# Kernel tuning notes

Measured on AMD Instinct MI355X. Metric: run time of the kernel, lower is better.

The kernel has to match this reference:

```python
import jax, jax.numpy as jnp
import numpy as np


def setup_inputs() -> dict:
    key = jax.random.key(0)
    k1, k2 = jax.random.split(key)
    B, C, H, W = 1, 128, 96, 128
    feat_l = jax.random.normal(k1, (B, C, H, W), dtype=jnp.float32)
    feat_r = jax.random.normal(k2, (B, C, H, W), dtype=jnp.float32)
    return {"feat_l": feat_l, "feat_r": feat_r, "scale_x": 4, "scale_y": 4}


def reference(feat_l, feat_r, scale_x, scale_y):
    B, C, H, W = feat_l.shape
    _, _, H_R, W_R = feat_r.shape
    # Full correlation volume: [B, H, W, H_R*W_R]  (the huge intermediate)
    corr = jnp.einsum('bchw,bcij->bhwij', feat_l, feat_r).reshape(B, H, W, H_R * W_R)
    flow_cost = jnp.max(corr, axis=3)           # [B, H, W]
    flat_idx = jnp.argmax(corr, axis=3)         # [B, H, W] int
    # Decode argmax index -> flow (u, v) relative to pixel grid
    xoff = jnp.arange(W)                        # [W]
    yoff = jnp.arange(H)                        # [H]
    u = -((flat_idx % W_R) * scale_x - xoff[None, None, :]).astype(jnp.float32)
    v = -((flat_idx // W_R) * scale_y - yoff[None, :, None]).astype(jnp.float32)
    flow = jnp.stack([u, v], axis=3)            # [B, H, W, 2]
    return flow, flow_cost
```

## Files before the change

### kernel.cpp

```cpp
#include <hip/hip_runtime.h>

#define K_TOT 128
#define H_DIM 96
#define W_DIM 128
#define M_TOT (H_DIM * W_DIM)
#define N_TOT (H_DIM * W_DIM)
#define SCALE 4
#define NEG_INF (-3.402823e38f)

#define KP 384
#define NH 24
#define SLAB_F16 24576

typedef _Float16 f16x8 __attribute__((ext_vector_type(8)));
typedef float f32x16 __attribute__((ext_vector_type(16)));

__global__ __launch_bounds__(256)
void split_prep_kernel(const float* __restrict__ L, const float* __restrict__ R,
                       _Float16* __restrict__ Ls, _Float16* __restrict__ Rs,
                       unsigned long long* __restrict__ keys) {
    const int t = threadIdx.x;
    if (blockIdx.x >= 1536) {
        int m = (blockIdx.x - 1536) * 256 + t;
        if (m < M_TOT) keys[m] = 0ull;
        return;
    }
    __shared__ __align__(16) _Float16 T[3][64][40];
    const int isR  = blockIdx.x >= 768;
    const int bb   = blockIdx.x - (isR ? 768 : 0);
    const int slab = bb >> 2;
    const int q    = bb & 3;
    const int P0   = slab * 64;
    const int kq   = q * 32;
    const float* src = isR ? R : L;
    _Float16* dst = isR ? Rs : Ls;

    const int p4 = (t & 15) * 4;
    const int k0 = t >> 4;
#pragma unroll
    for (int it = 0; it < 2; ++it) {
        const int kl = k0 + it * 16;
        float4 v = *(const float4*)&src[(size_t)(kq + kl) * M_TOT + P0 + p4];
        float xs[4] = {v.x, v.y, v.z, v.w};
#pragma unroll
        for (int j = 0; j < 4; ++j) {
            _Float16 h = (_Float16)xs[j];
            float hf = (float)h;
            float r = xs[j] - hf;
            T[0][p4 + j][kl] = h;
            T[1][p4 + j][kl] = (_Float16)(r * 64.0f);
            T[2][p4 + j][kl] = (_Float16)(hf * 0.015625f);
        }
    }
    __syncthreads();
#pragma unroll
    for (int it = 0; it < 3; ++it) {
        const int u   = it * 256 + t;
        const int col = u & 31;
        const int hi  = (u >> 5) & 1;
        const int op  = (u >> 6) & 1;
        const int jj  = (u >> 7) & 1;
        const int sec = u >> 8;
        const int half   = sec * 8 + 2 * q + jj;
        const int c      = half * 128 + op * 64 + hi * 32 + col;
        const int klocal = jj * 16 + hi * 8;
        const int plane  = (sec == 0) ? 0 : (isR ? sec : 3 - sec);
        const int row    = op * 32 + col;
        float4 v = *(const float4*)&T[plane][row][klocal];
        *(float4*)&dst[(size_t)slab * SLAB_F16 + (size_t)c * 8] = v;
    }
}

__global__ __launch_bounds__(256, 4)
void mfma_corr_kernel(const _Float16* __restrict__ Ls, const _Float16* __restrict__ Rs,
                      unsigned long long* __restrict__ keys) {
    __shared__ float vals[128 * 17];
    __shared__ int   idxs[128 * 17];

    const int tid  = threadIdx.x;
    const int lane = tid & 63;
    const int wid  = tid >> 6;
    const int wr   = wid >> 1;
    const int wc   = wid & 1;
    const int col  = lane & 31;
    const int hi   = lane >> 5;
    const int bid  = blockIdx.x;
    const int xcd  = bid & 7;
    const int b    = bid >> 3;
    const int mt   = b / 12;
    const int nt   = xcd * 12 + b % 12;
    const int m0   = mt * 128;
    const int n0   = nt * 128;

    const _Float16* pA = Ls + (size_t)(mt * 2 + wr) * SLAB_F16 + lane * 8;
    const _Float16* pB = Rs + (size_t)(nt * 2 + wc) * SLAB_F16 + lane * 8;

    f32x16 acc[2][2];
#pragma unroll
    for (int mi = 0; mi < 2; ++mi)
#pragma unroll
        for (int ni = 0; ni < 2; ++ni) acc[mi][ni] = (f32x16)(0.0f);

    f16x8 fA[3][2], fB[3][2];
#define LOADH(hh, s) {                                              \
        fA[s][0] = *(const f16x8*)(pA + (hh) * 1024);               \
        fA[s][1] = *(const f16x8*)(pA + (hh) * 1024 + 512);         \
        fB[s][0] = *(const f16x8*)(pB + (hh) * 1024);               \
        fB[s][1] = *(const f16x8*)(pB + (hh) * 1024 + 512);         \
    }
    LOADH(0, 0);
    LOADH(1, 1);
#pragma unroll
    for (int h = 0; h < NH; ++h) {
        if (h + 2 < NH) LOADH(h + 2, (h + 2) % 3);
        const int s = h % 3;
        __builtin_amdgcn_s_setprio(1);
        acc[0][0] = __builtin_amdgcn_mfma_f32_32x32x16_f16(fA[s][0], fB[s][0], acc[0][0], 0, 0, 0);
        acc[0][1] = __builtin_amdgcn_mfma_f32_32x32x16_f16(fA[s][0], fB[s][1], acc[0][1], 0, 0, 0);
        acc[1][0] = __builtin_amdgcn_mfma_f32_32x32x16_f16(fA[s][1], fB[s][0], acc[1][0], 0, 0, 0);
        acc[1][1] = __builtin_amdgcn_mfma_f32_32x32x16_f16(fA[s][1], fB[s][1], acc[1][1], 0, 0, 0);
        __builtin_amdgcn_s_setprio(0);
    }
#undef LOADH

#pragma unroll
    for (int mi = 0; mi < 2; ++mi) {
#pragma unroll
        for (int reg = 0; reg < 16; ++reg) {
            float best = acc[mi][0][reg];
            int bni = 0;
            if (acc[mi][1][reg] > best) { best = acc[mi][1][reg]; bni = 1; }
            int n = n0 + wc * 64 + bni * 32 + col;
#pragma unroll
            for (int d = 16; d >= 8; d >>= 1) {
                float ov = __shfl_xor(best, d, 64);
                int   oi = __shfl_xor(n, d, 64);
                if (ov > best || (ov == best && oi < n)) { best = ov; n = oi; }
            }
            if ((lane & 24) == 0) {
                const int row = wr * 64 + mi * 32 + (reg & 3) + 8 * (reg >> 2) + 4 * hi;
                const int c   = wc * 8 + (lane & 7);
                vals[row * 17 + c] = best;
                idxs[row * 17 + c] = n;
            }
        }
    }
    __syncthreads();
    if (tid < 128) {
        float bv = vals[tid * 17 + 0]; int bi = idxs[tid * 17 + 0];
#pragma unroll
        for (int c = 1; c < 16; ++c) {
            float v = vals[tid * 17 + c]; int ix = idxs[tid * 17 + c];
            if (v > bv || (v == bv && ix < bi)) { bv = v; bi = ix; }
        }
        unsigned vb = __float_as_uint(bv);
        vb = (vb & 0x80000000u) ? ~vb : (vb | 0x80000000u);
        unsigned long long key = ((unsigned long long)vb << 32) | (unsigned)(~bi);
        atomicMax(&keys[m0 + tid], key);
    }
}

__global__ void finalize_keys_kernel(const unsigned long long* __restrict__ keys,
                                     float* __restrict__ out) {
    int m = blockIdx.x * blockDim.x + threadIdx.x;
    if (m >= M_TOT) return;
    unsigned long long key = keys[m];
    unsigned hi = (unsigned)(key >> 32);
    unsigned bits = (hi & 0x80000000u) ? (hi & 0x7fffffffu) : ~hi;
    float v = __uint_as_float(bits);
    int idx = (int)(~(unsigned)(key & 0xffffffffu));
    int h = m / W_DIM, w = m % W_DIM;
    int i = idx / W_DIM, j = idx % W_DIM;
    out[m * 2 + 0] = (float)(w - SCALE * j);
    out[m * 2 + 1] = (float)(h - SCALE * i);
    out[2 * M_TOT + m] = v;
}

#define BM 128
#define BN 128
#define KB 32
__global__ __launch_bounds__(256)
void corr_argmax_kernel(const float* __restrict__ L, const float* __restrict__ R,
                        float* __restrict__ pbest, int* __restrict__ pidx,
                        int nsplit) {
    __shared__ float As[KB][BM];
    __shared__ float Bs[KB][BN];
    const int tid = threadIdx.x;
    const int mtiles = M_TOT / BM;
    const int mt = blockIdx.x % mtiles;
    const int s  = blockIdx.x / mtiles;
    const int m0 = mt * BM;
    const int ns = N_TOT / nsplit;
    const int ntiles = ns / BN;
    const int tx = tid & 15;
    const int ty = tid >> 4;
    float rbest[8]; int ridx[8];
#pragma unroll
    for (int i = 0; i < 8; ++i) { rbest[i] = NEG_INF; ridx[i] = 0; }
    for (int nt = 0; nt < ntiles; ++nt) {
        const int n0 = s * ns + nt * BN;
        float acc[8][8];
#pragma unroll
        for (int i = 0; i < 8; ++i)
#pragma unroll
            for (int j = 0; j < 8; ++j) acc[i][j] = 0.f;
        for (int kb = 0; kb < K_TOT; kb += KB) {
            __syncthreads();
#pragma unroll
            for (int r = 0; r < 4; ++r) {
                int f  = tid + 256 * r;
                int kk = f >> 5;
                int c4 = f & 31;
                float4 va = *reinterpret_cast<const float4*>(&L[(size_t)(kb + kk) * M_TOT + m0 + c4 * 4]);
                *reinterpret_cast<float4*>(&As[kk][c4 * 4]) = va;
                float4 vb = *reinterpret_cast<const float4*>(&R[(size_t)(kb + kk) * N_TOT + n0 + c4 * 4]);
                *reinterpret_cast<float4*>(&Bs[kk][c4 * 4]) = vb;
            }
            __syncthreads();
#pragma unroll 4
            for (int kk = 0; kk < KB; ++kk) {
                float4 a0 = *reinterpret_cast<const float4*>(&As[kk][ty * 4]);
                float4 a1 = *reinterpret_cast<const float4*>(&As[kk][64 + ty * 4]);
                float4 b0 = *reinterpret_cast<const float4*>(&Bs[kk][tx * 4]);
                float4 b1 = *reinterpret_cast<const float4*>(&Bs[kk][64 + tx * 4]);
                float a[8] = {a0.x, a0.y, a0.z, a0.w, a1.x, a1.y, a1.z, a1.w};
                float b[8] = {b0.x, b0.y, b0.z, b0.w, b1.x, b1.y, b1.z, b1.w};
#pragma unroll
                for (int i = 0; i < 8; ++i)
#pragma unroll
                    for (int j = 0; j < 8; ++j)
                        acc[i][j] = fmaf(a[i], b[j], acc[i][j]);
            }
        }
#pragma unroll
        for (int i = 0; i < 8; ++i)
#pragma unroll
            for (int jh = 0; jh < 2; ++jh)
#pragma unroll
                for (int jj = 0; jj < 4; ++jj) {
                    int n = n0 + jh * 64 + tx * 4 + jj;
                    float v = acc[i][jh * 4 + jj];
                    if (v > rbest[i]) { rbest[i] = v; ridx[i] = n; }
                }
    }
    __syncthreads();
    float (*redv)[BM] = reinterpret_cast<float(*)[BM]>(&As[0][0]);
    int   (*redi)[BM] = reinterpret_cast<int  (*)[BM]>(&Bs[0][0]);
#pragma unroll
    for (int i = 0; i < 8; ++i) {
        int row = (i >> 2) * 64 + ty * 4 + (i & 3);
        redv[tx][row] = rbest[i];
        redi[tx][row] = ridx[i];
    }
    __syncthreads();
    if (tid < BM) {
        float bv = NEG_INF; int bi = 0x7fffffff;
        for (int t = 0; t < 16; ++t) {
            float v  = redv[t][tid];
            int   ix = redi[t][tid];
            if (v > bv || (v == bv && ix < bi)) { bv = v; bi = ix; }
        }
        pbest[(size_t)s * M_TOT + m0 + tid] = bv;
        pidx [(size_t)s * M_TOT + m0 + tid] = bi;
    }
}

__global__ void finalize_parts_kernel(const float* __restrict__ pbest,
                                      const int* __restrict__ pidx,
                                      float* __restrict__ out, int nsplit) {
    int m = blockIdx.x * blockDim.x + threadIdx.x;
    if (m >= M_TOT) return;
    float bv = NEG_INF; int bi = 0x7fffffff;
    for (int s = 0; s < nsplit; ++s) {
        float v  = pbest[(size_t)s * M_TOT + m];
        int   ix = pidx [(size_t)s * M_TOT + m];
        if (v > bv || (v == bv && ix < bi)) { bv = v; bi = ix; }
    }
    int h = m / W_DIM, w = m % W_DIM;
    int i = bi / W_DIM, j = bi % W_DIM;
    out[m * 2 + 0] = (float)(w - SCALE * j);
    out[m * 2 + 1] = (float)(h - SCALE * i);
    out[2 * M_TOT + m] = bv;
}

extern "C" void kernel_launch(void* const* d_in, const int* in_sizes, int n_in,
                              void* d_out, int out_size, void* d_ws, size_t ws_size,
                              hipStream_t stream) {
    const float* L = (const float*)d_in[0];
    const float* R = (const float*)d_in[1];
    float* out = (float*)d_out;

    const size_t PKbytes = (size_t)M_TOT * KP * sizeof(_Float16);
    const size_t need = 2 * PKbytes + (size_t)M_TOT * 8;
    if (ws_size >= need) {
        _Float16* Ls = (_Float16*)d_ws;
        _Float16* Rs = (_Float16*)((char*)d_ws + PKbytes);
        unsigned long long* keys = (unsigned long long*)((char*)d_ws + 2 * PKbytes);
        split_prep_kernel<<<dim3(1584), dim3(256), 0, stream>>>(L, R, Ls, Rs, keys);
        mfma_corr_kernel<<<dim3((M_TOT / 128) * (N_TOT / 128)), dim3(256), 0, stream>>>(Ls, Rs, keys);
        finalize_keys_kernel<<<dim3(48), dim3(256), 0, stream>>>(keys, out);
    } else {
        int nsplit = 8;
        while (nsplit > 1 && (size_t)nsplit * M_TOT * 8 > ws_size) nsplit >>= 1;
        float* pbest = (float*)d_ws;
        int*   pidx  = (int*)((char*)d_ws + (size_t)nsplit * M_TOT * sizeof(float));
        corr_argmax_kernel<<<dim3((M_TOT / BM) * nsplit), dim3(256), 0, stream>>>(L, R, pbest, pidx, nsplit);
        finalize_parts_kernel<<<dim3((M_TOT + 255) / 256), dim3(256), 0, stream>>>(pbest, pidx, out, nsplit);
    }
}
```

Before: 225.0 us.

## Keep A tile resident in LDS and stream N tiles with register-held running argmax

Each block now loads a 64-row A slab into LDS once using async global-to-LDS loads. Its four waves then loop over 12 N-tiles of B read from global, keeping a per-register running max and packed tile code instead of reducing after every tile. The grid drops from many 128x128 tiles to 768 blocks, so there are fewer atomics and fewer epilogue reductions, and A reuse improves. In exchange the block holds 48KB of LDS with lower occupancy, each A fragment is re-read from LDS, and the running-argmax bookkeeping adds register pressure.

```diff
diff --git a/kernel.cpp b/kernel.cpp
--- a/kernel.cpp
+++ b/kernel.cpp
@@ -9,11 +9,15 @@
 #define NEG_INF (-3.402823e38f)
 
 #define KP 384
-#define NH 24
 #define SLAB_F16 24576
 
 typedef _Float16 f16x8 __attribute__((ext_vector_type(8)));
 typedef float f32x16 __attribute__((ext_vector_type(16)));
+
+#define ASYNC16(lds_ptr, g_ptr) \
+  __builtin_amdgcn_global_load_lds( \
+      (const __attribute__((address_space(1))) unsigned int*)(g_ptr), \
+      (__attribute__((address_space(3))) unsigned int*)(lds_ptr), 16, 0, 0)
 
 __global__ __launch_bounds__(256)
 void split_prep_kernel(const float* __restrict__ L, const float* __restrict__ R,
@@ -71,29 +75,34 @@
     }
 }
 
-__global__ __launch_bounds__(256, 4)
+__global__ __launch_bounds__(256, 3)
 void mfma_corr_kernel(const _Float16* __restrict__ Ls, const _Float16* __restrict__ Rs,
                       unsigned long long* __restrict__ keys) {
-    __shared__ float vals[128 * 17];
-    __shared__ int   idxs[128 * 17];
+    __shared__ __align__(16) char smem[49152];
 
     const int tid  = threadIdx.x;
     const int lane = tid & 63;
     const int wid  = tid >> 6;
-    const int wr   = wid >> 1;
-    const int wc   = wid & 1;
     const int col  = lane & 31;
     const int hi   = lane >> 5;
     const int bid  = blockIdx.x;
     const int xcd  = bid & 7;
-    const int b    = bid >> 3;
-    const int mt   = b / 12;
-    const int nt   = xcd * 12 + b % 12;
-    const int m0   = mt * 128;
-    const int n0   = nt * 128;
-
-    const _Float16* pA = Ls + (size_t)(mt * 2 + wr) * SLAB_F16 + lane * 8;
-    const _Float16* pB = Rs + (size_t)(nt * 2 + wc) * SLAB_F16 + lane * 8;
+    const int q    = xcd & 3;
+    const int mt   = ((bid >> 3) << 1) + (xcd >> 2);
+    const int m0   = mt * 64;
+
+#pragma unroll
+    for (int i = 0; i < 12; ++i) {
+        const int chunk = wid * 12 + i;
+        ASYNC16(smem + chunk * 1024,
+                Ls + (size_t)mt * SLAB_F16 + chunk * 512 + lane * 8);
+    }
+    __syncthreads();
+
+    float    rbv[32];
+    unsigned rcw[8] = {0, 0, 0, 0, 0, 0, 0, 0};
+#pragma unroll
+    for (int e = 0; e < 32; ++e) rbv[e] = NEG_INF;
 
     f32x16 acc[2][2];
 #pragma unroll
@@ -101,36 +110,66 @@
 #pragma unroll
         for (int ni = 0; ni < 2; ++ni) acc[mi][ni] = (f32x16)(0.0f);
 
-    f16x8 fA[3][2], fB[3][2];
-#define LOADH(hh, s) {                                              \
-        fA[s][0] = *(const f16x8*)(pA + (hh) * 1024);               \
-        fA[s][1] = *(const f16x8*)(pA + (hh) * 1024 + 512);         \
-        fB[s][0] = *(const f16x8*)(pB + (hh) * 1024);               \
-        fB[s][1] = *(const f16x8*)(pB + (hh) * 1024 + 512);         \
-    }
-    LOADH(0, 0);
-    LOADH(1, 1);
-#pragma unroll
-    for (int h = 0; h < NH; ++h) {
-        if (h + 2 < NH) LOADH(h + 2, (h + 2) % 3);
-        const int s = h % 3;
-        __builtin_amdgcn_s_setprio(1);
-        acc[0][0] = __builtin_amdgcn_mfma_f32_32x32x16_f16(fA[s][0], fB[s][0], acc[0][0], 0, 0, 0);
-        acc[0][1] = __builtin_amdgcn_mfma_f32_32x32x16_f16(fA[s][0], fB[s][1], acc[0][1], 0, 0, 0);
-        acc[1][0] = __builtin_amdgcn_mfma_f32_32x32x16_f16(fA[s][1], fB[s][0], acc[1][0], 0, 0, 0);
-        acc[1][1] = __builtin_amdgcn_mfma_f32_32x32x16_f16(fA[s][1], fB[s][1], acc[1][1], 0, 0, 0);
-        __builtin_amdgcn_s_setprio(0);
-    }
-#undef LOADH
-
-#pragma unroll
-    for (int mi = 0; mi < 2; ++mi) {
+    const _Float16* pB = Rs + (size_t)(q * 48 + wid) * SLAB_F16 + lane * 8;
+    f16x8 fB[3][2];
+    fB[0][0] = *(const f16x8*)(pB);
+    fB[0][1] = *(const f16x8*)(pB + 512);
+    fB[1][0] = *(const f16x8*)(pB + 1024);
+    fB[1][1] = *(const f16x8*)(pB + 1536);
+
+    for (int j = 0; j < 12; ++j) {
+        const _Float16* pBn = pB + (size_t)4 * SLAB_F16;
+#pragma unroll
+        for (int h = 0; h < 24; ++h) {
+            if (j < 11 || h < 22) {
+                const _Float16* ps = (h < 22) ? (pB + (h + 2) * 1024)
+                                              : (pBn + (h - 22) * 1024);
+                const int s2 = (h + 2) % 3;
+                fB[s2][0] = *(const f16x8*)(ps);
+                fB[s2][1] = *(const f16x8*)(ps + 512);
+            }
+            const int s = h % 3;
+            f16x8 a0 = *(const f16x8*)(smem + h * 2048 + lane * 16);
+            f16x8 a1 = *(const f16x8*)(smem + h * 2048 + 1024 + lane * 16);
+            __builtin_amdgcn_s_setprio(1);
+            acc[0][0] = __builtin_amdgcn_mfma_f32_32x32x16_f16(a0, fB[s][0], acc[0][0], 0, 0, 0);
+            acc[0][1] = __builtin_amdgcn_mfma_f32_32x32x16_f16(a0, fB[s][1], acc[0][1], 0, 0, 0);
+            acc[1][0] = __builtin_amdgcn_mfma_f32_32x32x16_f16(a1, fB[s][0], acc[1][0], 0, 0, 0);
+            acc[1][1] = __builtin_amdgcn_mfma_f32_32x32x16_f16(a1, fB[s][1], acc[1][1], 0, 0, 0);
+            __builtin_amdgcn_s_setprio(0);
+        }
+        const unsigned cj = (unsigned)(j << 1);
+#pragma unroll
+        for (int mi = 0; mi < 2; ++mi)
+#pragma unroll
+            for (int reg = 0; reg < 16; ++reg) {
+                const int e = mi * 16 + reg;
+                float v0 = acc[mi][0][reg], v1 = acc[mi][1][reg];
+                const bool sel = v1 > v0;
+                float v = sel ? v1 : v0;
+                unsigned code = cj | (sel ? 1u : 0u);
+                if (v > rbv[e]) {
+                    rbv[e] = v;
+                    const int w = e >> 2, sh = (e & 3) * 8;
+                    rcw[w] = (rcw[w] & ~(255u << sh)) | (code << sh);
+                }
+                acc[mi][0][reg] = 0.0f;
+                acc[mi][1][reg] = 0.0f;
+            }
+        pB = pBn;
+    }
+
+    __syncthreads();
+    float* vals = (float*)smem;
+    int*   idxs = (int*)(smem + 8448);
+#pragma unroll
+    for (int mi = 0; mi < 2; ++mi)
 #pragma unroll
         for (int reg = 0; reg < 16; ++reg) {
-            float best = acc[mi][0][reg];
-            int bni = 0;
-            if (acc[mi][1][reg] > best) { best = acc[mi][1][reg]; bni = 1; }
-            int n = n0 + wc * 64 + bni * 32 + col;
+            const int e = mi * 16 + reg;
+            float best = rbv[e];
+            const unsigned code = (rcw[e >> 2] >> ((e & 3) * 8)) & 255u;
+            int n = (q * 48 + wid + 4 * (int)(code >> 1)) * 64 + (int)(code & 1) * 32 + col;
 #pragma unroll
             for (int d = 16; d >= 8; d >>= 1) {
                 float ov = __shfl_xor(best, d, 64);
@@ -138,19 +177,18 @@
                 if (ov > best || (ov == best && oi < n)) { best = ov; n = oi; }
             }
             if ((lane & 24) == 0) {
-                const int row = wr * 64 + mi * 32 + (reg & 3) + 8 * (reg >> 2) + 4 * hi;
-                const int c   = wc * 8 + (lane & 7);
-                vals[row * 17 + c] = best;
-                idxs[row * 17 + c] = n;
-            }
-        }
-    }
-    __syncthreads();
-    if (tid < 128) {
-        float bv = vals[tid * 17 + 0]; int bi = idxs[tid * 17 + 0];
-#pragma unroll
-        for (int c = 1; c < 16; ++c) {
-            float v = vals[tid * 17 + c]; int ix = idxs[tid * 17 + c];
+                const int row = mi * 32 + (reg & 3) + 8 * (reg >> 2) + 4 * hi;
+                const int c   = wid * 8 + (lane & 7);
+                vals[row * 33 + c] = best;
+                idxs[row * 33 + c] = n;
+            }
+        }
+    __syncthreads();
+    if (tid < 64) {
+        float bv = vals[tid * 33 + 0]; int bi = idxs[tid * 33 + 0];
+#pragma unroll
+        for (int c = 1; c < 32; ++c) {
+            float v = vals[tid * 33 + c]; int ix = idxs[tid * 33 + c];
             if (v > bv || (v == bv && ix < bi)) { bv = v; bi = ix; }
         }
         unsigned vb = __float_as_uint(bv);
@@ -297,7 +335,7 @@
         _Float16* Rs = (_Float16*)((char*)d_ws + PKbytes);
         unsigned long long* keys = (unsigned long long*)((char*)d_ws + 2 * PKbytes);
         split_prep_kernel<<<dim3(1584), dim3(256), 0, stream>>>(L, R, Ls, Rs, keys);
-        mfma_corr_kernel<<<dim3((M_TOT / 128) * (N_TOT / 128)), dim3(256), 0, stream>>>(Ls, Rs, keys);
+        mfma_corr_kernel<<<dim3(768), dim3(256), 0, stream>>>(Ls, Rs, keys);
         finalize_keys_kernel<<<dim3(48), dim3(256), 0, stream>>>(keys, out);
     } else {
         int nsplit = 8;
```

Measured after the change: 387.9 us. 72.4% more time.
